# Performance work log

Measured on AMD Instinct MI355X. Metric: run time of the kernel, lower is better.

The kernel has to match this reference:

```python
import jax, jax.numpy as jnp
import numpy as np

TREE_DEPTH = 4
N_LEAVES = 2 ** TREE_DEPTH      # 16
N_INTERNAL = 2 ** TREE_DEPTH - 1  # 15
TEMP = 1.0
EPS = 1e-5


def _build_paths(depth):
    nl = 2 ** depth
    pi = np.zeros((nl, depth), np.int32)
    pd = np.zeros((nl, depth), np.float32)
    for leaf in range(nl):
        node = 0
        for d in range(depth):
            pi[leaf, d] = node
            bit = (leaf >> (depth - 1 - d)) & 1
            pd[leaf, d] = 1.0 - bit
            node = 2 * node + 1 + bit
    return jnp.asarray(pi), jnp.asarray(pd)

PATH_IDX, PATH_DIR = _build_paths(TREE_DEPTH)


def setup_inputs() -> dict:
    key = jax.random.key(0)
    k0, k1, k2, k3 = jax.random.split(key, 4)
    B, S, D, O, T = 4, 2048, 1024, 512, 16
    x = jax.random.normal(k0, (B, S, D), jnp.float32)
    decision_weights = 0.1 * jax.random.normal(k1, (T, N_INTERNAL, D), jnp.float32)
    decision_biases = jnp.zeros((T, N_INTERNAL), jnp.float32)
    xavier = float(np.sqrt(2.0 / (N_LEAVES + O)))
    leaf_outputs = xavier * jax.random.normal(k2, (T, N_LEAVES, O), jnp.float32)
    gate_w = 0.02 * jax.random.normal(k3, (D, T), jnp.float32)
    gate_b = jnp.zeros((T,), jnp.float32)
    node_temp_logits = jnp.zeros((T, N_INTERNAL), jnp.float32)
    ln_gamma = jnp.ones((O,), jnp.float32)
    ln_beta = jnp.zeros((O,), jnp.float32)
    return dict(x=x, decision_weights=decision_weights, decision_biases=decision_biases,
                leaf_outputs=leaf_outputs, gate_w=gate_w, gate_b=gate_b,
                node_temp_logits=node_temp_logits, ln_gamma=ln_gamma, ln_beta=ln_beta)


def reference(x, decision_weights, decision_biases, leaf_outputs,
              gate_w, gate_b, node_temp_logits, ln_gamma, ln_beta):
    # decision logits: (B,S,T,N)
    logits = jnp.einsum('bsd,tnd->bstn', x, decision_weights) + decision_biases
    # per-node learnable temperature (softplus(0.5413) ~= 1)
    node_temps = TEMP * jax.nn.softplus(node_temp_logits + 0.5413)
    decisions = jax.nn.sigmoid(logits / node_temps)
    # gather decisions along each root->leaf path: (B,S,T,L,depth)
    relevant = decisions[..., PATH_IDX]
    probs_per_level = PATH_DIR * relevant + (1.0 - PATH_DIR) * (1.0 - relevant)
    leaf_probs = jnp.prod(probs_per_level, axis=-1)  # (B,S,T,L)
    per_tree = jnp.einsum('bstl,tlo->bsto', leaf_probs, leaf_outputs)
    gate = jax.nn.softmax(x @ gate_w + gate_b, axis=-1)  # (B,S,T)
    out = jnp.einsum('bsto,bst->bso', per_tree, gate)
    # LayerNorm over last dim
    mu = jnp.mean(out, axis=-1, keepdims=True)
    var = jnp.var(out, axis=-1, keepdims=True)
    return (out - mu) / jnp.sqrt(var + EPS) * ln_gamma + ln_beta
```

## Files before the change

kernel.cpp:

```cpp
#include <hip/hip_runtime.h>
#include <math.h>

#define TOK 8192
#define DD  1024
#define OO  512
#define NC  256

#define WC4_HI 0
#define WC4_LO (512*1024)
#define LO4_HI (1024*1024)
#define LO4_LO (1280*1024)
#define PAR_B  (1536*1024)

typedef __attribute__((ext_vector_type(8))) short short8;
typedef __attribute__((ext_vector_type(4))) float f32x4;

#define MFMA16(a,b,c) __builtin_amdgcn_mfma_f32_16x16x32_bf16((a),(b),(c),0,0,0)

__device__ __forceinline__ ushort f2bh(float f) {
  union { float f; unsigned u; } v; v.f = f;
  unsigned r = v.u + 0x7fffu + ((v.u >> 16) & 1u);
  return (ushort)(r >> 16);
}
__device__ __forceinline__ float bh2f(ushort h) {
  union { unsigned u; float f; } v; v.u = ((unsigned)h) << 16; return v.f;
}
__device__ __forceinline__ void split2(float f, ushort& h, ushort& l) {
  h = f2bh(f);
  l = f2bh(f - bh2f(h));
}

__global__ __launch_bounds__(256) void k_prep(
    const float* __restrict__ dw, const float* __restrict__ db,
    const float* __restrict__ lo_in, const float* __restrict__ gw,
    const float* __restrict__ ntl, char* __restrict__ ws) {
  const int bid = blockIdx.x, tid = threadIdx.x;
  if (bid < 128) {
    const int idx  = bid * 256 + tid;
    const int k8   = idx >> 8;
    const int ncol = idx & 255;
    float v[8];
    if (ncol < 240) {
#pragma unroll
      for (int c = 0; c < 8; ++c) v[c] = dw[(size_t)ncol * DD + k8 * 8 + c];
    } else {
      const int t = ncol - 240;
#pragma unroll
      for (int c = 0; c < 8; ++c) v[c] = gw[(size_t)(k8 * 8 + c) * 16 + t];
    }
    short8 h, l;
#pragma unroll
    for (int e = 0; e < 8; ++e) {
      ushort hh, ll; split2(v[e], hh, ll);
      h[e] = (short)hh; l[e] = (short)ll;
    }
    const size_t o16 = ((size_t)k8 * 256 + ncol) * 16;
    *(short8*)(ws + WC4_HI + o16) = h;
    *(short8*)(ws + WC4_LO + o16) = l;
  } else if (bid < 192) {
    const int idx  = (bid - 128) * 256 + tid;
    const int k8   = idx >> 9;
    const int ocol = idx & 511;
    float v[8];
#pragma unroll
    for (int c = 0; c < 8; ++c) v[c] = lo_in[(size_t)(k8 * 8 + c) * OO + ocol];
    short8 h, l;
#pragma unroll
    for (int e = 0; e < 8; ++e) {
      ushort hh, ll; split2(v[e], hh, ll);
      h[e] = (short)hh; l[e] = (short)ll;
    }
    const size_t o16 = ((size_t)k8 * 512 + ocol) * 16;
    *(short8*)(ws + LO4_HI + o16) = h;
    *(short8*)(ws + LO4_LO + o16) = l;
  } else {
    if (tid < 240) {
      float v = ntl[tid] + 0.5413f;
      float sp = (v > 20.f) ? v : log1pf(expf(v));
      float* par = (float*)(ws + PAR_B);
      par[tid]       = db[tid];
      par[240 + tid] = 1.0f / sp;
    }
  }
}

#define XSB(b)  ((b) * 16384)
#define ACT_B   0
#define WF_HI   33280
#define WF_LO   49664
#define SM_SZ   66048

__global__ __launch_bounds__(512) void k_fused(
    const float* __restrict__ x, const char* __restrict__ ws,
    const float* __restrict__ gate_b, const float* __restrict__ gamma,
    const float* __restrict__ beta, float* __restrict__ out) {
  __shared__ __align__(16) char sm[SM_SZ];

  const char* wc4_hi = ws + WC4_HI;
  const char* wc4_lo = ws + WC4_LO;
  const char* lo4_hi = ws + LO4_HI;
  const char* lo4_lo = ws + LO4_LO;
  const float* par   = (const float*)(ws + PAR_B);

  const int tid  = threadIdx.x;
  const int wv   = tid >> 6;
  const int lane = tid & 63;
  const int l15  = lane & 15;
  const int kgrp = lane >> 4;
  const int m0   = blockIdx.x * 32;

  f32x4 acc00 = {0,0,0,0}, acc01 = {0,0,0,0}, acc10 = {0,0,0,0}, acc11 = {0,0,0,0};
  short8 ah0, ah1, al0, al1;
  short8 bhE[2], blE[2], bhO[2], blO[2];
  float4 pxa, pxb;

  auto xload = [&](int CH) {
    const int m_ = tid >> 5, kl = (tid & 31) << 2;
    pxa = *(const float4*)&x[(size_t)(m0 + m_) * DD + CH * 128 + kl];
    pxb = *(const float4*)&x[(size_t)(m0 + 16 + m_) * DD + CH * 128 + kl];
  };
  auto xstore = [&](int BUF) {
    const int kl2 = ((tid & 31) << 2) * 2;
    ushort4 h, l;
    split2(pxa.x, h.x, l.x); split2(pxa.y, h.y, l.y);
    split2(pxa.z, h.z, l.z); split2(pxa.w, h.w, l.w);
    {
      const int m_ = tid >> 5;
      const int off = (m_ * 256 + kl2) ^ ((m_ & 7) << 4);
      *(ushort4*)(sm + XSB(BUF) + off) = h;
      *(ushort4*)(sm + XSB(BUF) + 8192 + off) = l;
    }
    split2(pxb.x, h.x, l.x); split2(pxb.y, h.y, l.y);
    split2(pxb.z, h.z, l.z); split2(pxb.w, h.w, l.w);
    {
      const int m_ = 16 + (tid >> 5);
      const int off = (m_ * 256 + kl2) ^ ((m_ & 7) << 4);
      *(ushort4*)(sm + XSB(BUF) + off) = h;
      *(ushort4*)(sm + XSB(BUF) + 8192 + off) = l;
    }
  };
  auto loadB1 = [&](int F, short8 (&BH)[2], short8 (&BL)[2]) {
    const size_t base = ((size_t)(F * 4 + kgrp) * 256) * 16;
#pragma unroll
    for (int j = 0; j < 2; ++j) {
      const size_t o = base + (size_t)(wv * 32 + j * 16 + l15) * 16;
      BH[j] = *(const short8*)(wc4_hi + o);
      BL[j] = *(const short8*)(wc4_lo + o);
    }
  };
  auto afrag = [&](int CB, int KS) {
    const int k0 = KS * 64 + kgrp * 16;
    const int a0 = (l15 * 256 + k0) ^ ((l15 & 7) << 4);
    const int a1 = ((16 + l15) * 256 + k0) ^ ((l15 & 7) << 4);
    ah0 = *(const short8*)(sm + XSB(CB) + a0);
    al0 = *(const short8*)(sm + XSB(CB) + 8192 + a0);
    ah1 = *(const short8*)(sm + XSB(CB) + a1);
    al1 = *(const short8*)(sm + XSB(CB) + 8192 + a1);
  };
  auto mfmaStep = [&](short8 (&BH)[2], short8 (&BL)[2]) {
    acc00 = MFMA16(ah0, BH[0], acc00); acc00 = MFMA16(ah0, BL[0], acc00);
    acc00 = MFMA16(al0, BH[0], acc00);
    acc01 = MFMA16(ah0, BH[1], acc01); acc01 = MFMA16(ah0, BL[1], acc01);
    acc01 = MFMA16(al0, BH[1], acc01);
    acc10 = MFMA16(ah1, BH[0], acc10); acc10 = MFMA16(ah1, BL[0], acc10);
    acc10 = MFMA16(al1, BH[0], acc10);
    acc11 = MFMA16(ah1, BH[1], acc11); acc11 = MFMA16(ah1, BL[1], acc11);
    acc11 = MFMA16(al1, BH[1], acc11);
  };

  xload(0);
  xstore(0);
  loadB1(0, bhE, blE);

  for (int ch = 0; ch < 8; ++ch) {
    __syncthreads();
    const int cb = ch & 1;
    if (ch < 7) xload(ch + 1);
    const int f = ch * 4;
    afrag(cb, 0); loadB1(f + 1, bhO, blO); mfmaStep(bhE, blE);
    afrag(cb, 1); loadB1(f + 2, bhE, blE); mfmaStep(bhO, blO);
    afrag(cb, 2); loadB1(f + 3, bhO, blO); mfmaStep(bhE, blE);
    afrag(cb, 3); loadB1((f + 4 < 32) ? f + 4 : 31, bhE, blE); mfmaStep(bhO, blO);
    if (ch < 7) xstore(cb ^ 1);
  }
  __syncthreads();

  {
    const f32x4 a[2][2] = {{acc00, acc01}, {acc10, acc11}};
#pragma unroll
    for (int mi = 0; mi < 2; ++mi)
#pragma unroll
      for (int j = 0; j < 2; ++j)
#pragma unroll
        for (int r = 0; r < 4; ++r) {
          const int row = mi * 16 + kgrp * 4 + r;
          const int col = wv * 32 + j * 16 + l15;
          *(float*)(sm + ACT_B + (row * 260 + col) * 4) = a[mi][j][r];
        }
  }
  __syncthreads();

  short8 cbhE[4], cblE[4], cbhO[4], cblO[4];
  auto loadB2 = [&](int F, short8 (&BH)[4], short8 (&BL)[4]) {
    const size_t base = ((size_t)(F * 4 + kgrp) * 512) * 16;
#pragma unroll
    for (int t = 0; t < 4; ++t) {
      const size_t o = base + (size_t)(wv * 64 + t * 16 + l15) * 16;
      BH[t] = *(const short8*)(lo4_hi + o);
      BL[t] = *(const short8*)(lo4_lo + o);
    }
  };
  loadB2(0, cbhE, cblE);

  {
    const int token = tid >> 4;
    const int tr    = tid & 15;
    const float* arow_p = (const float*)(sm + ACT_B + token * 260 * 4);

    float dec[15];
#pragma unroll
    for (int i = 0; i < 15; ++i) {
      const int ci = tr * 15 + i;
      const float z = (arow_p[ci] + par[ci]) * par[240 + ci];
      dec[i] = 1.f / (1.f + expf(-z));
    }
    float gl = arow_p[240 + tr] + gate_b[tr];
    float gmax = gl;
#pragma unroll
    for (int msk = 8; msk >= 1; msk >>= 1) gmax = fmaxf(gmax, __shfl_xor(gmax, msk, 16));
    const float ge = expf(gl - gmax);
    float gsum = ge;
#pragma unroll
    for (int msk = 8; msk >= 1; msk >>= 1) gsum += __shfl_xor(gsum, msk, 16);
    const float gate = ge / gsum;

    float lp[16];
#pragma unroll
    for (int l = 0; l < 16; ++l) {
      float p = gate;
      int node = 0;
#pragma unroll
      for (int d = 0; d < 4; ++d) {
        const int bit = (l >> (3 - d)) & 1;
        p *= bit ? (1.f - dec[node]) : dec[node];
        node = 2 * node + 1 + bit;
      }
      lp[l] = p;
    }
    short8 h0, h1, l0, l1;
#pragma unroll
    for (int e = 0; e < 8; ++e) {
      ushort hh, ll;
      split2(lp[e], hh, ll);     h0[e] = (short)hh; l0[e] = (short)ll;
      split2(lp[8 + e], hh, ll); h1[e] = (short)hh; l1[e] = (short)ll;
    }
    const int b0 = (token * 512 + tr * 32) ^ ((token & 7) << 4);
    const int b1 = (token * 512 + tr * 32 + 16) ^ ((token & 7) << 4);
    *(short8*)(sm + WF_HI + b0) = h0;
    *(short8*)(sm + WF_HI + b1) = h1;
    *(short8*)(sm + WF_LO + b0) = l0;
    *(short8*)(sm + WF_LO + b1) = l1;
  }
  __syncthreads();

  f32x4 ac0[4], ac1[4];
#pragma unroll
  for (int t = 0; t < 4; ++t) { ac0[t] = (f32x4){0,0,0,0}; ac1[t] = (f32x4){0,0,0,0}; }
  short8 wah0, wah1, wal0, wal1;
  auto wafrag = [&](int FC) {
    const int k0 = FC * 64 + kgrp * 16;
    const int a0 = (l15 * 512 + k0) ^ ((l15 & 7) << 4);
    const int a1 = ((16 + l15) * 512 + k0) ^ ((l15 & 7) << 4);
    wah0 = *(const short8*)(sm + WF_HI + a0);
    wal0 = *(const short8*)(sm + WF_LO + a0);
    wah1 = *(const short8*)(sm + WF_HI + a1);
    wal1 = *(const short8*)(sm + WF_LO + a1);
  };
  auto mfma2Step = [&](short8 (&BH)[4], short8 (&BL)[4]) {
#pragma unroll
    for (int t = 0; t < 4; ++t) {
      ac0[t] = MFMA16(wah0, BH[t], ac0[t]); ac0[t] = MFMA16(wah0, BL[t], ac0[t]);
      ac0[t] = MFMA16(wal0, BH[t], ac0[t]);
      ac1[t] = MFMA16(wah1, BH[t], ac1[t]); ac1[t] = MFMA16(wah1, BL[t], ac1[t]);
      ac1[t] = MFMA16(wal1, BH[t], ac1[t]);
    }
  };

#pragma unroll
  for (int it = 0; it < 4; ++it) {
    const int fe = it * 2;
    wafrag(fe);     loadB2(fe + 1, cbhO, cblO);                 mfma2Step(cbhE, cblE);
    wafrag(fe + 1); loadB2((fe + 2 < 8) ? fe + 2 : 7, cbhE, cblE); mfma2Step(cbhO, cblO);
  }

  float* ps = (float*)sm;
#pragma unroll
  for (int mi = 0; mi < 2; ++mi)
#pragma unroll
    for (int r = 0; r < 4; ++r) {
      float s = 0.f, q = 0.f;
#pragma unroll
      for (int t = 0; t < 4; ++t) {
        const float v = (mi == 0) ? ac0[t][r] : ac1[t][r];
        s += v; q += v * v;
      }
#pragma unroll
      for (int msk = 8; msk >= 1; msk >>= 1) {
        s += __shfl_xor(s, msk, 16);
        q += __shfl_xor(q, msk, 16);
      }
      if (l15 == 0) {
        const int row = mi * 16 + kgrp * 4 + r;
        ps[(row * 8 + wv) * 2 + 0] = s;
        ps[(row * 8 + wv) * 2 + 1] = q;
      }
    }
  __syncthreads();

#pragma unroll
  for (int mi = 0; mi < 2; ++mi)
#pragma unroll
    for (int r = 0; r < 4; ++r) {
      const int row = mi * 16 + kgrp * 4 + r;
      float S = 0.f, Q = 0.f;
#pragma unroll
      for (int p = 0; p < 8; ++p) {
        S += ps[(row * 8 + p) * 2 + 0];
        Q += ps[(row * 8 + p) * 2 + 1];
      }
      const float mu  = S * (1.f / 512.f);
      const float var = Q * (1.f / 512.f) - mu * mu;
      const float rs  = rsqrtf(var + 1e-5f);
#pragma unroll
      for (int t = 0; t < 4; ++t) {
        const int col = wv * 64 + t * 16 + l15;
        const float v = (mi == 0) ? ac0[t][r] : ac1[t][r];
        out[(size_t)(m0 + row) * OO + col] = (v - mu) * rs * gamma[col] + beta[col];
      }
    }
}

extern "C" void kernel_launch(void* const* d_in, const int* in_sizes, int n_in,
                              void* d_out, int out_size, void* d_ws, size_t ws_size,
                              hipStream_t stream) {
  const float* x   = (const float*)d_in[0];
  const float* dw  = (const float*)d_in[1];
  const float* db  = (const float*)d_in[2];
  const float* lo  = (const float*)d_in[3];
  const float* gw  = (const float*)d_in[4];
  const float* gb  = (const float*)d_in[5];
  const float* ntl = (const float*)d_in[6];
  const float* g   = (const float*)d_in[7];
  const float* b   = (const float*)d_in[8];
  char* ws   = (char*)d_ws;
  float* out = (float*)d_out;

  k_prep<<<193, 256, 0, stream>>>(dw, db, lo, gw, ntl, ws);
  k_fused<<<256, 512, 0, stream>>>(x, ws, gb, g, b, out);
}
```

Baseline: 121.7 us.

## Double token tile per block to 64 rows and transpose weight prep through LDS

The fused kernel now processes 64 tokens per block instead of 32, so each loaded weight fragment feeds twice as many MFMAs and weight traffic per token halves. The launch grid drops to 128 blocks and LDS use doubles to 128 KB, which lowers occupancy and leaves fewer blocks than CUs. The prep kernel also transposes decision weights through shared memory with coalesced float4 loads instead of strided scalar reads.

```diff
diff --git a/kernel.cpp b/kernel.cpp
--- a/kernel.cpp
+++ b/kernel.cpp
@@ -35,30 +35,45 @@
     const float* __restrict__ lo_in, const float* __restrict__ gw,
     const float* __restrict__ ntl, char* __restrict__ ws) {
   const int bid = blockIdx.x, tid = threadIdx.x;
-  if (bid < 128) {
-    const int idx  = bid * 256 + tid;
-    const int k8   = idx >> 8;
-    const int ncol = idx & 255;
-    float v[8];
-    if (ncol < 240) {
-#pragma unroll
-      for (int c = 0; c < 8; ++c) v[c] = dw[(size_t)ncol * DD + k8 * 8 + c];
-    } else {
-      const int t = ncol - 240;
-#pragma unroll
-      for (int c = 0; c < 8; ++c) v[c] = gw[(size_t)(k8 * 8 + c) * 16 + t];
-    }
-    short8 h, l;
-#pragma unroll
-    for (int e = 0; e < 8; ++e) {
-      ushort hh, ll; split2(v[e], hh, ll);
-      h[e] = (short)hh; l[e] = (short)ll;
-    }
-    const size_t o16 = ((size_t)k8 * 256 + ncol) * 16;
-    *(short8*)(ws + WC4_HI + o16) = h;
-    *(short8*)(ws + WC4_LO + o16) = l;
-  } else if (bid < 192) {
-    const int idx  = (bid - 128) * 256 + tid;
+  if (bid < 16) {
+    __shared__ char pt[65536];
+    const int n0 = (bid & 3) * 64;
+    const int k0 = (bid >> 2) * 256;
+    const int kl4 = (tid & 63) << 2;
+#pragma unroll
+    for (int i = 0; i < 16; ++i) {
+      const int row = (tid >> 6) + 4 * i;
+      const int n = n0 + row;
+      float v[4];
+      if (n < 240) {
+        const float4 t4 = *(const float4*)&dw[(size_t)n * DD + k0 + kl4];
+        v[0] = t4.x; v[1] = t4.y; v[2] = t4.z; v[3] = t4.w;
+      } else {
+        const int t = n - 240;
+#pragma unroll
+        for (int c = 0; c < 4; ++c) v[c] = gw[(size_t)(k0 + kl4 + c) * 16 + t];
+      }
+      ushort4 h, l;
+      split2(v[0], h.x, l.x); split2(v[1], h.y, l.y);
+      split2(v[2], h.z, l.z); split2(v[3], h.w, l.w);
+      const int u = kl4 >> 3, half = (kl4 >> 2) & 1;
+      const int boff = row * 512 + ((u ^ (row & 31)) << 4) + half * 8;
+      *(ushort4*)(pt + boff) = h;
+      *(ushort4*)(pt + 32768 + boff) = l;
+    }
+    __syncthreads();
+#pragma unroll
+    for (int j = 0; j < 8; ++j) {
+      const int u = tid + 256 * j;
+      const int c = u & 63;
+      const int kk = u >> 6;
+      const int src = c * 512 + ((kk ^ (c & 31)) << 4);
+      const size_t dst = ((size_t)((k0 >> 3) + kk) * 256 + n0 + c) * 16;
+      *(short8*)(ws + WC4_HI + dst) = *(const short8*)(pt + src);
+      *(short8*)(ws + WC4_LO + dst) = *(const short8*)(pt + 32768 + src);
+    }
+  } else if (bid < 80) {
+    const int idx  = (bid - 16) * 256 + tid;
     const int k8   = idx >> 9;
     const int ocol = idx & 511;
     float v[8];
@@ -84,13 +99,12 @@
   }
 }
 
-#define XSB(b)  ((b) * 16384)
-#define ACT_B   0
-#define WF_HI   33280
-#define WF_LO   49664
-#define SM_SZ   66048
-
-__global__ __launch_bounds__(512) void k_fused(
+#define XSB(b)  ((b) * 32768)
+#define WF_HI   65536
+#define WF_LO   98304
+#define SM_SZ   131072
+
+__global__ __launch_bounds__(512, 2) void k_fused(
     const float* __restrict__ x, const char* __restrict__ ws,
     const float* __restrict__ gate_b, const float* __restrict__ gamma,
     const float* __restrict__ beta, float* __restrict__ out) {
@@ -107,36 +121,35 @@
   const int lane = tid & 63;
   const int l15  = lane & 15;
   const int kgrp = lane >> 4;
-  const int m0   = blockIdx.x * 32;
-
-  f32x4 acc00 = {0,0,0,0}, acc01 = {0,0,0,0}, acc10 = {0,0,0,0}, acc11 = {0,0,0,0};
-  short8 ah0, ah1, al0, al1;
+  const int m0   = blockIdx.x * 64;
+
+  f32x4 acc[4][2];
+#pragma unroll
+  for (int mt = 0; mt < 4; ++mt)
+#pragma unroll
+    for (int j = 0; j < 2; ++j) acc[mt][j] = (f32x4){0, 0, 0, 0};
+  short8 ah[4], al[4];
   short8 bhE[2], blE[2], bhO[2], blO[2];
-  float4 pxa, pxb;
+  float4 px[4];
+
+  const int xm = tid >> 5;
+  const int xk = (tid & 31) << 2;
 
   auto xload = [&](int CH) {
-    const int m_ = tid >> 5, kl = (tid & 31) << 2;
-    pxa = *(const float4*)&x[(size_t)(m0 + m_) * DD + CH * 128 + kl];
-    pxb = *(const float4*)&x[(size_t)(m0 + 16 + m_) * DD + CH * 128 + kl];
+#pragma unroll
+    for (int rr = 0; rr < 4; ++rr)
+      px[rr] = *(const float4*)&x[(size_t)(m0 + rr * 16 + xm) * DD + CH * 128 + xk];
   };
   auto xstore = [&](int BUF) {
-    const int kl2 = ((tid & 31) << 2) * 2;
-    ushort4 h, l;
-    split2(pxa.x, h.x, l.x); split2(pxa.y, h.y, l.y);
-    split2(pxa.z, h.z, l.z); split2(pxa.w, h.w, l.w);
-    {
-      const int m_ = tid >> 5;
-      const int off = (m_ * 256 + kl2) ^ ((m_ & 7) << 4);
+#pragma unroll
+    for (int rr = 0; rr < 4; ++rr) {
+      ushort4 h, l;
+      split2(px[rr].x, h.x, l.x); split2(px[rr].y, h.y, l.y);
+      split2(px[rr].z, h.z, l.z); split2(px[rr].w, h.w, l.w);
+      const int row = rr * 16 + xm;
+      const int off = (row * 256 + xk * 2) ^ ((row & 7) << 4);
       *(ushort4*)(sm + XSB(BUF) + off) = h;
-      *(ushort4*)(sm + XSB(BUF) + 8192 + off) = l;
-    }
-    split2(pxb.x, h.x, l.x); split2(pxb.y, h.y, l.y);
-    split2(pxb.z, h.z, l.z); split2(pxb.w, h.w, l.w);
-    {
-      const int m_ = 16 + (tid >> 5);
-      const int off = (m_ * 256 + kl2) ^ ((m_ & 7) << 4);
-      *(ushort4*)(sm + XSB(BUF) + off) = h;
-      *(ushort4*)(sm + XSB(BUF) + 8192 + off) = l;
+      *(ushort4*)(sm + XSB(BUF) + 16384 + off) = l;
     }
   };
   auto loadB1 = [&](int F, short8 (&BH)[2], short8 (&BL)[2]) {
@@ -149,23 +162,24 @@
     }
   };
   auto afrag = [&](int CB, int KS) {
-    const int k0 = KS * 64 + kgrp * 16;
-    const int a0 = (l15 * 256 + k0) ^ ((l15 & 7) << 4);
-    const int a1 = ((16 + l15) * 256 + k0) ^ ((l15 & 7) << 4);
-    ah0 = *(const short8*)(sm + XSB(CB) + a0);
-    al0 = *(const short8*)(sm + XSB(CB) + 8192 + a0);
-    ah1 = *(const short8*)(sm + XSB(CB) + a1);
-    al1 = *(const short8*)(sm + XSB(CB) + 8192 + a1);
+    const int k0b = KS * 64 + kgrp * 16;
+#pragma unroll
+    for (int mt = 0; mt < 4; ++mt) {
+      const int row = mt * 16 + l15;
+      const int a = (row * 256 + k0b) ^ ((row & 7) << 4);
+      ah[mt] = *(const short8*)(sm + XSB(CB) + a);
+      al[mt] = *(const short8*)(sm + XSB(CB) + 16384 + a);
+    }
   };
   auto mfmaStep = [&](short8 (&BH)[2], short8 (&BL)[2]) {
-    acc00 = MFMA16(ah0, BH[0], acc00); acc00 = MFMA16(ah0, BL[0], acc00);
-    acc00 = MFMA16(al0, BH[0], acc00);
-    acc01 = MFMA16(ah0, BH[1], acc01); acc01 = MFMA16(ah0, BL[1], acc01);
-    acc01 = MFMA16(al0, BH[1], acc01);
-    acc10 = MFMA16(ah1, BH[0], acc10); acc10 = MFMA16(ah1, BL[0], acc10);
-    acc10 = MFMA16(al1, BH[0], acc10);
-    acc11 = MFMA16(ah1, BH[1], acc11); acc11 = MFMA16(ah1, BL[1], acc11);
-    acc11 = MFMA16(al1, BH[1], acc11);
+#pragma unroll
+    for (int mt = 0; mt < 4; ++mt)
+#pragma unroll
+      for (int j = 0; j < 2; ++j) {
+        acc[mt][j] = MFMA16(ah[mt], BH[j], acc[mt][j]);
+        acc[mt][j] = MFMA16(ah[mt], BL[j], acc[mt][j]);
+        acc[mt][j] = MFMA16(al[mt], BH[j], acc[mt][j]);
+      }
   };
 
   xload(0);
@@ -186,16 +200,16 @@
   __syncthreads();
 
   {
-    const f32x4 a[2][2] = {{acc00, acc01}, {acc10, acc11}};
-#pragma unroll
-    for (int mi = 0; mi < 2; ++mi)
+    float* actp = (float*)sm;
+#pragma unroll
+    for (int mt = 0; mt < 4; ++mt)
 #pragma unroll
       for (int j = 0; j < 2; ++j)
 #pragma unroll
         for (int r = 0; r < 4; ++r) {
-          const int row = mi * 16 + kgrp * 4 + r;
+          const int row = mt * 16 + kgrp * 4 + r;
           const int col = wv * 32 + j * 16 + l15;
-          *(float*)(sm + ACT_B + (row * 260 + col) * 4) = a[mi][j][r];
+          actp[row * 256 + col] = acc[mt][j][r];
         }
   }
   __syncthreads();
@@ -213,95 +227,103 @@
   loadB2(0, cbhE, cblE);
 
   {
-    const int token = tid >> 4;
-    const int tr    = tid & 15;
-    const float* arow_p = (const float*)(sm + ACT_B + token * 260 * 4);
-
-    float dec[15];
-#pragma unroll
-    for (int i = 0; i < 15; ++i) {
-      const int ci = tr * 15 + i;
-      const float z = (arow_p[ci] + par[ci]) * par[240 + ci];
-      dec[i] = 1.f / (1.f + expf(-z));
-    }
-    float gl = arow_p[240 + tr] + gate_b[tr];
-    float gmax = gl;
-#pragma unroll
-    for (int msk = 8; msk >= 1; msk >>= 1) gmax = fmaxf(gmax, __shfl_xor(gmax, msk, 16));
-    const float ge = expf(gl - gmax);
-    float gsum = ge;
-#pragma unroll
-    for (int msk = 8; msk >= 1; msk >>= 1) gsum += __shfl_xor(gsum, msk, 16);
-    const float gate = ge / gsum;
-
-    float lp[16];
-#pragma unroll
-    for (int l = 0; l < 16; ++l) {
-      float p = gate;
-      int node = 0;
-#pragma unroll
-      for (int d = 0; d < 4; ++d) {
-        const int bit = (l >> (3 - d)) & 1;
-        p *= bit ? (1.f - dec[node]) : dec[node];
-        node = 2 * node + 1 + bit;
-      }
-      lp[l] = p;
-    }
-    short8 h0, h1, l0, l1;
-#pragma unroll
-    for (int e = 0; e < 8; ++e) {
-      ushort hh, ll;
-      split2(lp[e], hh, ll);     h0[e] = (short)hh; l0[e] = (short)ll;
-      split2(lp[8 + e], hh, ll); h1[e] = (short)hh; l1[e] = (short)ll;
-    }
-    const int b0 = (token * 512 + tr * 32) ^ ((token & 7) << 4);
-    const int b1 = (token * 512 + tr * 32 + 16) ^ ((token & 7) << 4);
-    *(short8*)(sm + WF_HI + b0) = h0;
-    *(short8*)(sm + WF_HI + b1) = h1;
-    *(short8*)(sm + WF_LO + b0) = l0;
-    *(short8*)(sm + WF_LO + b1) = l1;
+    const float* actp = (const float*)sm;
+    const int tr = tid & 15;
+#pragma unroll
+    for (int p = 0; p < 2; ++p) {
+      const int token = p * 32 + (tid >> 4);
+      const float* arow_p = actp + token * 256;
+
+      float dec[15];
+#pragma unroll
+      for (int i = 0; i < 15; ++i) {
+        const int ci = tr * 15 + i;
+        const float z = (arow_p[ci] + par[ci]) * par[240 + ci];
+        dec[i] = 1.f / (1.f + expf(-z));
+      }
+      float gl = arow_p[240 + tr] + gate_b[tr];
+      float gmax = gl;
+#pragma unroll
+      for (int msk = 8; msk >= 1; msk >>= 1) gmax = fmaxf(gmax, __shfl_xor(gmax, msk, 16));
+      const float ge = expf(gl - gmax);
+      float gsum = ge;
+#pragma unroll
+      for (int msk = 8; msk >= 1; msk >>= 1) gsum += __shfl_xor(gsum, msk, 16);
+      const float gate = ge / gsum;
+
+      float lp[16];
+#pragma unroll
+      for (int l = 0; l < 16; ++l) {
+        float pp = gate;
+        int node = 0;
+#pragma unroll
+        for (int d = 0; d < 4; ++d) {
+          const int bit = (l >> (3 - d)) & 1;
+          pp *= bit ? (1.f - dec[node]) : dec[node];
+          node = 2 * node + 1 + bit;
+        }
+        lp[l] = pp;
+      }
+      short8 h0, h1, l0, l1;
+#pragma unroll
+      for (int e = 0; e < 8; ++e) {
+        ushort hh, ll;
+        split2(lp[e], hh, ll);     h0[e] = (short)hh; l0[e] = (short)ll;
+        split2(lp[8 + e], hh, ll); h1[e] = (short)hh; l1[e] = (short)ll;
+      }
+      const int b0 = (token * 512 + tr * 32) ^ ((token & 7) << 4);
+      const int b1 = (token * 512 + tr * 32 + 16) ^ ((token & 7) << 4);
+      *(short8*)(sm + WF_HI + b0) = h0;
+      *(short8*)(sm + WF_HI + b1) = h1;
+      *(short8*)(sm + WF_LO + b0) = l0;
+      *(short8*)(sm + WF_LO + b1) = l1;
+    }
   }
   __syncthreads();
 
-  f32x4 ac0[4], ac1[4];
-#pragma unroll
-  for (int t = 0; t < 4; ++t) { ac0[t] = (f32x4){0,0,0,0}; ac1[t] = (f32x4){0,0,0,0}; }
-  short8 wah0, wah1, wal0, wal1;
+  f32x4 acc2[4][4];
+#pragma unroll
+  for (int mt = 0; mt < 4; ++mt)
+#pragma unroll
+    for (int t = 0; t < 4; ++t) acc2[mt][t] = (f32x4){0, 0, 0, 0};
+  short8 wah[4], wal[4];
   auto wafrag = [&](int FC) {
-    const int k0 = FC * 64 + kgrp * 16;
-    const int a0 = (l15 * 512 + k0) ^ ((l15 & 7) << 4);
-    const int a1 = ((16 + l15) * 512 + k0) ^ ((l15 & 7) << 4);
-    wah0 = *(const short8*)(sm + WF_HI + a0);
-    wal0 = *(const short8*)(sm + WF_LO + a0);
-    wah1 = *(const short8*)(sm + WF_HI + a1);
-    wal1 = *(const short8*)(sm + WF_LO + a1);
+    const int k0b = FC * 64 + kgrp * 16;
+#pragma unroll
+    for (int mt = 0; mt < 4; ++mt) {
+      const int row = mt * 16 + l15;
+      const int a = (row * 512 + k0b) ^ ((row & 7) << 4);
+      wah[mt] = *(const short8*)(sm + WF_HI + a);
+      wal[mt] = *(const short8*)(sm + WF_LO + a);
+    }
   };
   auto mfma2Step = [&](short8 (&BH)[4], short8 (&BL)[4]) {
 #pragma unroll
-    for (int t = 0; t < 4; ++t) {
-      ac0[t] = MFMA16(wah0, BH[t], ac0[t]); ac0[t] = MFMA16(wah0, BL[t], ac0[t]);
-      ac0[t] = MFMA16(wal0, BH[t], ac0[t]);
-      ac1[t] = MFMA16(wah1, BH[t], ac1[t]); ac1[t] = MFMA16(wah1, BL[t], ac1[t]);
-      ac1[t] = MFMA16(wal1, BH[t], ac1[t]);
-    }
+    for (int mt = 0; mt < 4; ++mt)
+#pragma unroll
+      for (int t = 0; t < 4; ++t) {
+        acc2[mt][t] = MFMA16(wah[mt], BH[t], acc2[mt][t]);
+        acc2[mt][t] = MFMA16(wah[mt], BL[t], acc2[mt][t]);
+        acc2[mt][t] = MFMA16(wal[mt], BH[t], acc2[mt][t]);
+      }
   };
 
 #pragma unroll
   for (int it = 0; it < 4; ++it) {
     const int fe = it * 2;
-    wafrag(fe);     loadB2(fe + 1, cbhO, cblO);                 mfma2Step(cbhE, cblE);
+    wafrag(fe);     loadB2(fe + 1, cbhO, cblO);                    mfma2Step(cbhE, cblE);
     wafrag(fe + 1); loadB2((fe + 2 < 8) ? fe + 2 : 7, cbhE, cblE); mfma2Step(cbhO, cblO);
   }
 
   float* ps = (float*)sm;
 #pragma unroll
-  for (int mi = 0; mi < 2; ++mi)
+  for (int mt = 0; mt < 4; ++mt)
 #pragma unroll
     for (int r = 0; r < 4; ++r) {
       float s = 0.f, q = 0.f;
 #pragma unroll
       for (int t = 0; t < 4; ++t) {
-        const float v = (mi == 0) ? ac0[t][r] : ac1[t][r];
+        const float v = acc2[mt][t][r];
         s += v; q += v * v;
       }
 #pragma unroll
@@ -310,7 +332,7 @@
         q += __shfl_xor(q, msk, 16);
       }
       if (l15 == 0) {
-        const int row = mi * 16 + kgrp * 4 + r;
+        const int row = mt * 16 + kgrp * 4 + r;
         ps[(row * 8 + wv) * 2 + 0] = s;
         ps[(row * 8 + wv) * 2 + 1] = q;
       }
@@ -318,10 +340,10 @@
   __syncthreads();
 
 #pragma unroll
-  for (int mi = 0; mi < 2; ++mi)
+  for (int mt = 0; mt < 4; ++mt)
 #pragma unroll
     for (int r = 0; r < 4; ++r) {
-      const int row = mi * 16 + kgrp * 4 + r;
+      const int row = mt * 16 + kgrp * 4 + r;
       float S = 0.f, Q = 0.f;
 #pragma unroll
       for (int p = 0; p < 8; ++p) {
@@ -334,8 +356,8 @@
 #pragma unroll
       for (int t = 0; t < 4; ++t) {
         const int col = wv * 64 + t * 16 + l15;
-        const float v = (mi == 0) ? ac0[t][r] : ac1[t][r];
-        out[(size_t)(m0 + row) * OO + col] = (v - mu) * rs * gamma[col] + beta[col];
+        out[(size_t)(m0 + row) * OO + col] =
+            (acc2[mt][t][r] - mu) * rs * gamma[col] + beta[col];
       }
     }
 }
@@ -355,6 +377,6 @@
   char* ws   = (char*)d_ws;
   float* out = (float*)d_out;
 
-  k_prep<<<193, 256, 0, stream>>>(dw, db, lo, gw, ntl, ws);
-  k_fused<<<256, 512, 0, stream>>>(x, ws, gb, g, b, out);
-}
+  k_prep<<<81, 256, 0, stream>>>(dw, db, lo, gw, ntl, ws);
+  k_fused<<<128, 512, 0, stream>>>(x, ws, gb, g, b, out);
+}
```

Measured after the change: 135.9 us. 11.7% more time.

## Deepen weight prefetch pipelines, transpose prep via LDS, widen swizzle

Applied to the files above, without the earlier changes.

The prep kernel now converts decision and gate weights using coalesced float4 loads into a shared-memory transpose tile, replacing strided scalar reads, with fewer blocks. The fused kernel prefetches B fragments two steps ahead (a 4-slot ring in GEMM1, a 3-slot ring in GEMM2) instead of one, to hide global load latency. It also widens the LDS XOR swizzle from 8 to 16 rows and drops the padded activation stride, which shrinks shared memory to exactly 64KB. The cost is more live registers, which may reduce occupancy or cause spills.

```diff
diff --git a/kernel.cpp b/kernel.cpp
--- a/kernel.cpp
+++ b/kernel.cpp
@@ -35,30 +35,45 @@
     const float* __restrict__ lo_in, const float* __restrict__ gw,
     const float* __restrict__ ntl, char* __restrict__ ws) {
   const int bid = blockIdx.x, tid = threadIdx.x;
-  if (bid < 128) {
-    const int idx  = bid * 256 + tid;
-    const int k8   = idx >> 8;
-    const int ncol = idx & 255;
-    float v[8];
-    if (ncol < 240) {
-#pragma unroll
-      for (int c = 0; c < 8; ++c) v[c] = dw[(size_t)ncol * DD + k8 * 8 + c];
-    } else {
-      const int t = ncol - 240;
-#pragma unroll
-      for (int c = 0; c < 8; ++c) v[c] = gw[(size_t)(k8 * 8 + c) * 16 + t];
-    }
-    short8 h, l;
-#pragma unroll
-    for (int e = 0; e < 8; ++e) {
-      ushort hh, ll; split2(v[e], hh, ll);
-      h[e] = (short)hh; l[e] = (short)ll;
-    }
-    const size_t o16 = ((size_t)k8 * 256 + ncol) * 16;
-    *(short8*)(ws + WC4_HI + o16) = h;
-    *(short8*)(ws + WC4_LO + o16) = l;
-  } else if (bid < 192) {
-    const int idx  = (bid - 128) * 256 + tid;
+  if (bid < 16) {
+    __shared__ char pt[65536];
+    const int n0 = (bid & 3) * 64;
+    const int k0 = (bid >> 2) * 256;
+    const int kl4 = (tid & 63) << 2;
+#pragma unroll
+    for (int i = 0; i < 16; ++i) {
+      const int row = (tid >> 6) + 4 * i;
+      const int n = n0 + row;
+      float v[4];
+      if (n < 240) {
+        const float4 t4 = *(const float4*)&dw[(size_t)n * DD + k0 + kl4];
+        v[0] = t4.x; v[1] = t4.y; v[2] = t4.z; v[3] = t4.w;
+      } else {
+        const int t = n - 240;
+#pragma unroll
+        for (int c = 0; c < 4; ++c) v[c] = gw[(size_t)(k0 + kl4 + c) * 16 + t];
+      }
+      ushort4 h, l;
+      split2(v[0], h.x, l.x); split2(v[1], h.y, l.y);
+      split2(v[2], h.z, l.z); split2(v[3], h.w, l.w);
+      const int u = kl4 >> 3, half = (kl4 >> 2) & 1;
+      const int boff = row * 512 + ((u ^ (row & 31)) << 4) + half * 8;
+      *(ushort4*)(pt + boff) = h;
+      *(ushort4*)(pt + 32768 + boff) = l;
+    }
+    __syncthreads();
+#pragma unroll
+    for (int j = 0; j < 8; ++j) {
+      const int u = tid + 256 * j;
+      const int c = u & 63;
+      const int kk = u >> 6;
+      const int src = c * 512 + ((kk ^ (c & 31)) << 4);
+      const size_t dst = ((size_t)((k0 >> 3) + kk) * 256 + n0 + c) * 16;
+      *(short8*)(ws + WC4_HI + dst) = *(const short8*)(pt + src);
+      *(short8*)(ws + WC4_LO + dst) = *(const short8*)(pt + 32768 + src);
+    }
+  } else if (bid < 80) {
+    const int idx  = (bid - 16) * 256 + tid;
     const int k8   = idx >> 9;
     const int ocol = idx & 511;
     float v[8];
@@ -85,10 +100,9 @@
 }
 
 #define XSB(b)  ((b) * 16384)
-#define ACT_B   0
-#define WF_HI   33280
-#define WF_LO   49664
-#define SM_SZ   66048
+#define WF_HI   32768
+#define WF_LO   49152
+#define SM_SZ   65536
 
 __global__ __launch_bounds__(512) void k_fused(
     const float* __restrict__ x, const char* __restrict__ ws,
@@ -111,7 +125,7 @@
 
   f32x4 acc00 = {0,0,0,0}, acc01 = {0,0,0,0}, acc10 = {0,0,0,0}, acc11 = {0,0,0,0};
   short8 ah0, ah1, al0, al1;
-  short8 bhE[2], blE[2], bhO[2], blO[2];
+  short8 b1h[4][2], b1l[4][2];
   float4 pxa, pxb;
 
   auto xload = [&](int CH) {
@@ -126,7 +140,7 @@
     split2(pxa.z, h.z, l.z); split2(pxa.w, h.w, l.w);
     {
       const int m_ = tid >> 5;
-      const int off = (m_ * 256 + kl2) ^ ((m_ & 7) << 4);
+      const int off = (m_ * 256 + kl2) ^ ((m_ & 15) << 4);
       *(ushort4*)(sm + XSB(BUF) + off) = h;
       *(ushort4*)(sm + XSB(BUF) + 8192 + off) = l;
     }
@@ -134,58 +148,61 @@
     split2(pxb.z, h.z, l.z); split2(pxb.w, h.w, l.w);
     {
       const int m_ = 16 + (tid >> 5);
-      const int off = (m_ * 256 + kl2) ^ ((m_ & 7) << 4);
+      const int off = (m_ * 256 + kl2) ^ ((m_ & 15) << 4);
       *(ushort4*)(sm + XSB(BUF) + off) = h;
       *(ushort4*)(sm + XSB(BUF) + 8192 + off) = l;
     }
   };
-  auto loadB1 = [&](int F, short8 (&BH)[2], short8 (&BL)[2]) {
-    const size_t base = ((size_t)(F * 4 + kgrp) * 256) * 16;
-#pragma unroll
-    for (int j = 0; j < 2; ++j) {
-      const size_t o = base + (size_t)(wv * 32 + j * 16 + l15) * 16;
-      BH[j] = *(const short8*)(wc4_hi + o);
-      BL[j] = *(const short8*)(wc4_lo + o);
-    }
-  };
+#define LOADB1(F, S) do {                                               \
+    const int Fc = (F) < 31 ? (F) : 31;                                 \
+    const size_t base = ((size_t)(Fc * 4 + kgrp) * 256) * 16;           \
+    _Pragma("unroll")                                                   \
+    for (int j = 0; j < 2; ++j) {                                       \
+      const size_t o = base + (size_t)(wv * 32 + j * 16 + l15) * 16;    \
+      b1h[S][j] = *(const short8*)(wc4_hi + o);                         \
+      b1l[S][j] = *(const short8*)(wc4_lo + o);                         \
+    }                                                                   \
+  } while (0)
   auto afrag = [&](int CB, int KS) {
     const int k0 = KS * 64 + kgrp * 16;
-    const int a0 = (l15 * 256 + k0) ^ ((l15 & 7) << 4);
-    const int a1 = ((16 + l15) * 256 + k0) ^ ((l15 & 7) << 4);
+    const int a0 = (l15 * 256 + k0) ^ ((l15 & 15) << 4);
+    const int a1 = ((16 + l15) * 256 + k0) ^ ((l15 & 15) << 4);
     ah0 = *(const short8*)(sm + XSB(CB) + a0);
     al0 = *(const short8*)(sm + XSB(CB) + 8192 + a0);
     ah1 = *(const short8*)(sm + XSB(CB) + a1);
     al1 = *(const short8*)(sm + XSB(CB) + 8192 + a1);
   };
-  auto mfmaStep = [&](short8 (&BH)[2], short8 (&BL)[2]) {
-    acc00 = MFMA16(ah0, BH[0], acc00); acc00 = MFMA16(ah0, BL[0], acc00);
-    acc00 = MFMA16(al0, BH[0], acc00);
-    acc01 = MFMA16(ah0, BH[1], acc01); acc01 = MFMA16(ah0, BL[1], acc01);
-    acc01 = MFMA16(al0, BH[1], acc01);
-    acc10 = MFMA16(ah1, BH[0], acc10); acc10 = MFMA16(ah1, BL[0], acc10);
-    acc10 = MFMA16(al1, BH[0], acc10);
-    acc11 = MFMA16(ah1, BH[1], acc11); acc11 = MFMA16(ah1, BL[1], acc11);
-    acc11 = MFMA16(al1, BH[1], acc11);
-  };
+#define MFMASTEP(S) do {                                                   \
+    acc00 = MFMA16(ah0, b1h[S][0], acc00); acc00 = MFMA16(ah0, b1l[S][0], acc00); \
+    acc00 = MFMA16(al0, b1h[S][0], acc00);                                 \
+    acc01 = MFMA16(ah0, b1h[S][1], acc01); acc01 = MFMA16(ah0, b1l[S][1], acc01); \
+    acc01 = MFMA16(al0, b1h[S][1], acc01);                                 \
+    acc10 = MFMA16(ah1, b1h[S][0], acc10); acc10 = MFMA16(ah1, b1l[S][0], acc10); \
+    acc10 = MFMA16(al1, b1h[S][0], acc10);                                 \
+    acc11 = MFMA16(ah1, b1h[S][1], acc11); acc11 = MFMA16(ah1, b1l[S][1], acc11); \
+    acc11 = MFMA16(al1, b1h[S][1], acc11);                                 \
+  } while (0)
 
   xload(0);
   xstore(0);
-  loadB1(0, bhE, blE);
+  LOADB1(0, 0);
+  LOADB1(1, 1);
 
   for (int ch = 0; ch < 8; ++ch) {
     __syncthreads();
     const int cb = ch & 1;
     if (ch < 7) xload(ch + 1);
     const int f = ch * 4;
-    afrag(cb, 0); loadB1(f + 1, bhO, blO); mfmaStep(bhE, blE);
-    afrag(cb, 1); loadB1(f + 2, bhE, blE); mfmaStep(bhO, blO);
-    afrag(cb, 2); loadB1(f + 3, bhO, blO); mfmaStep(bhE, blE);
-    afrag(cb, 3); loadB1((f + 4 < 32) ? f + 4 : 31, bhE, blE); mfmaStep(bhO, blO);
+    LOADB1(f + 2, 2); afrag(cb, 0); MFMASTEP(0);
+    LOADB1(f + 3, 3); afrag(cb, 1); MFMASTEP(1);
+    LOADB1(f + 4, 0); afrag(cb, 2); MFMASTEP(2);
+    LOADB1(f + 5, 1); afrag(cb, 3); MFMASTEP(3);
     if (ch < 7) xstore(cb ^ 1);
   }
   __syncthreads();
 
   {
+    float* actp = (float*)sm;
     const f32x4 a[2][2] = {{acc00, acc01}, {acc10, acc11}};
 #pragma unroll
     for (int mi = 0; mi < 2; ++mi)
@@ -195,27 +212,28 @@
         for (int r = 0; r < 4; ++r) {
           const int row = mi * 16 + kgrp * 4 + r;
           const int col = wv * 32 + j * 16 + l15;
-          *(float*)(sm + ACT_B + (row * 260 + col) * 4) = a[mi][j][r];
+          actp[row * 256 + col] = a[mi][j][r];
         }
   }
   __syncthreads();
 
-  short8 cbhE[4], cblE[4], cbhO[4], cblO[4];
-  auto loadB2 = [&](int F, short8 (&BH)[4], short8 (&BL)[4]) {
-    const size_t base = ((size_t)(F * 4 + kgrp) * 512) * 16;
-#pragma unroll
-    for (int t = 0; t < 4; ++t) {
-      const size_t o = base + (size_t)(wv * 64 + t * 16 + l15) * 16;
-      BH[t] = *(const short8*)(lo4_hi + o);
-      BL[t] = *(const short8*)(lo4_lo + o);
-    }
-  };
-  loadB2(0, cbhE, cblE);
+  short8 c2h[3][4], c2l[3][4];
+#define LOADB2(F, S) do {                                               \
+    const size_t base = ((size_t)((F) * 4 + kgrp) * 512) * 16;          \
+    _Pragma("unroll")                                                   \
+    for (int t = 0; t < 4; ++t) {                                       \
+      const size_t o = base + (size_t)(wv * 64 + t * 16 + l15) * 16;    \
+      c2h[S][t] = *(const short8*)(lo4_hi + o);                         \
+      c2l[S][t] = *(const short8*)(lo4_lo + o);                         \
+    }                                                                   \
+  } while (0)
+  LOADB2(0, 0);
 
   {
+    const float* actp = (const float*)sm;
     const int token = tid >> 4;
     const int tr    = tid & 15;
-    const float* arow_p = (const float*)(sm + ACT_B + token * 260 * 4);
+    const float* arow_p = actp + token * 256;
 
     float dec[15];
 #pragma unroll
@@ -254,8 +272,8 @@
       split2(lp[e], hh, ll);     h0[e] = (short)hh; l0[e] = (short)ll;
       split2(lp[8 + e], hh, ll); h1[e] = (short)hh; l1[e] = (short)ll;
     }
-    const int b0 = (token * 512 + tr * 32) ^ ((token & 7) << 4);
-    const int b1 = (token * 512 + tr * 32 + 16) ^ ((token & 7) << 4);
+    const int b0 = (token * 512 + tr * 32) ^ ((token & 15) << 4);
+    const int b1 = (token * 512 + tr * 32 + 16) ^ ((token & 15) << 4);
     *(short8*)(sm + WF_HI + b0) = h0;
     *(short8*)(sm + WF_HI + b1) = h1;
     *(short8*)(sm + WF_LO + b0) = l0;
@@ -269,29 +287,34 @@
   short8 wah0, wah1, wal0, wal1;
   auto wafrag = [&](int FC) {
     const int k0 = FC * 64 + kgrp * 16;
-    const int a0 = (l15 * 512 + k0) ^ ((l15 & 7) << 4);
-    const int a1 = ((16 + l15) * 512 + k0) ^ ((l15 & 7) << 4);
+    const int a0 = (l15 * 512 + k0) ^ ((l15 & 15) << 4);
+    const int a1 = ((16 + l15) * 512 + k0) ^ ((l15 & 15) << 4);
     wah0 = *(const short8*)(sm + WF_HI + a0);
     wal0 = *(const short8*)(sm + WF_LO + a0);
     wah1 = *(const short8*)(sm + WF_HI + a1);
     wal1 = *(const short8*)(sm + WF_LO + a1);
   };
-  auto mfma2Step = [&](short8 (&BH)[4], short8 (&BL)[4]) {
-#pragma unroll
-    for (int t = 0; t < 4; ++t) {
-      ac0[t] = MFMA16(wah0, BH[t], ac0[t]); ac0[t] = MFMA16(wah0, BL[t], ac0[t]);
-      ac0[t] = MFMA16(wal0, BH[t], ac0[t]);
-      ac1[t] = MFMA16(wah1, BH[t], ac1[t]); ac1[t] = MFMA16(wah1, BL[t], ac1[t]);
-      ac1[t] = MFMA16(wal1, BH[t], ac1[t]);
-    }
-  };
-
-#pragma unroll
-  for (int it = 0; it < 4; ++it) {
-    const int fe = it * 2;
-    wafrag(fe);     loadB2(fe + 1, cbhO, cblO);                 mfma2Step(cbhE, cblE);
-    wafrag(fe + 1); loadB2((fe + 2 < 8) ? fe + 2 : 7, cbhE, cblE); mfma2Step(cbhO, cblO);
-  }
+#define MFMA2STEP(S) do {                                                  \
+    _Pragma("unroll")                                                      \
+    for (int t = 0; t < 4; ++t) {                                          \
+      ac0[t] = MFMA16(wah0, c2h[S][t], ac0[t]);                            \
+      ac0[t] = MFMA16(wah0, c2l[S][t], ac0[t]);                            \
+      ac0[t] = MFMA16(wal0, c2h[S][t], ac0[t]);                            \
+      ac1[t] = MFMA16(wah1, c2h[S][t], ac1[t]);                            \
+      ac1[t] = MFMA16(wah1, c2l[S][t], ac1[t]);                            \
+      ac1[t] = MFMA16(wal1, c2h[S][t], ac1[t]);                            \
+    }                                                                      \
+  } while (0)
+
+  LOADB2(1, 1);
+  LOADB2(2, 2); wafrag(0); MFMA2STEP(0);
+  LOADB2(3, 0); wafrag(1); MFMA2STEP(1);
+  LOADB2(4, 1); wafrag(2); MFMA2STEP(2);
+  LOADB2(5, 2); wafrag(3); MFMA2STEP(0);
+  LOADB2(6, 0); wafrag(4); MFMA2STEP(1);
+  LOADB2(7, 1); wafrag(5); MFMA2STEP(2);
+  wafrag(6); MFMA2STEP(0);
+  wafrag(7); MFMA2STEP(1);
 
   float* ps = (float*)sm;
 #pragma unroll
@@ -355,6 +378,6 @@
   char* ws   = (char*)d_ws;
   float* out = (float*)d_out;
 
-  k_prep<<<193, 256, 0, stream>>>(dw, db, lo, gw, ntl, ws);
+  k_prep<<<81, 256, 0, stream>>>(dw, db, lo, gw, ntl, ws);
   k_fused<<<256, 512, 0, stream>>>(x, ws, gb, g, b, out);
 }
```

After: 124.3 us. +2.1%, slower.
